# Kernel optimization log

Hardware: AMD Instinct MI355X
Metric: run time of the kernel (lower is better)

## Reference

```python
import jax, jax.numpy as jnp
import numpy as np

B, T, E = 2, 2048, 2048
H, D = 16, 128
KVH = H // 2
THETA = 10000.0

def make_rope(dim, seq_len, theta):
    inv_freqs = 1.0 / (theta ** (jnp.arange(0, dim, 2, dtype=jnp.float32) / dim))
    positions = jnp.arange(seq_len, dtype=jnp.float32)
    freqs = positions[:, None] * inv_freqs[None, :]  # (T, D/2)
    return jax.lax.complex(jnp.cos(freqs), jnp.sin(freqs))

def apply_rope(x, rope):
    # x: (B, h, T, D), rope: (T, D/2) complex
    xr = x.astype(jnp.float32).reshape(*x.shape[:-1], -1, 2)
    xc = jax.lax.complex(xr[..., 0], xr[..., 1])
    out = xc * rope[None, None, :, :]
    return jnp.stack([jnp.real(out), jnp.imag(out)], axis=-1).reshape(x.shape).astype(x.dtype)

def setup_inputs() -> dict:
    key = jax.random.key(0)
    ks = jax.random.split(key, 5)
    x = jax.random.normal(ks[0], (B, T, E), dtype=jnp.float32)
    mask = jnp.tril(jnp.ones((T, T), dtype=jnp.int32))[None, None]  # causal (1,1,T,T)
    s = 0.02
    wq = jax.random.normal(ks[1], (E, H * D), dtype=jnp.float32) * s
    wk = jax.random.normal(ks[2], (E, KVH * D), dtype=jnp.float32) * s
    wv = jax.random.normal(ks[3], (E, KVH * D), dtype=jnp.float32) * s
    wo = jax.random.normal(ks[4], (H * D, E), dtype=jnp.float32) * s
    return {"x": x, "mask": mask, "wq": wq, "wk": wk, "wv": wv, "wo": wo}

def reference(x, mask, wq, wk, wv, wo):
    rope = make_rope(D, T, THETA)
    q = (x @ wq).reshape(B, T, H, D).transpose(0, 2, 1, 3)      # (B,H,T,D)
    k = (x @ wk).reshape(B, T, KVH, D).transpose(0, 2, 1, 3)    # (B,KVH,T,D)
    v = (x @ wv).reshape(B, T, KVH, D).transpose(0, 2, 1, 3)
    q = apply_rope(q, rope)
    k = apply_rope(k, rope)
    # GQA: repeat kv heads to match query heads
    k = jnp.repeat(k, H // KVH, axis=1)
    v = jnp.repeat(v, H // KVH, axis=1)
    scale = D ** -0.5
    attn = jnp.einsum('bhqd,bhkd->bhqk', q, k) * scale
    attn = jnp.where(mask == 0, -jnp.inf, attn)
    attn = jax.nn.softmax(attn, axis=-1)
    attn = jnp.where(jnp.isnan(attn), 0.0, attn)
    out = jnp.einsum('bhqk,bhkd->bhqd', attn, v)
    out = out.transpose(0, 2, 1, 3).reshape(B, T, H * D)
    return out @ wo
```

## Files before the change

### kernel.cpp

```cpp
#include <hip/hip_runtime.h>
#include <math.h>

#define Bb   2
#define Tt   2048
#define Ee   2048
#define Hh   16
#define KVHh 8
#define Dd   128
#define Mm   (Bb*Tt)

typedef unsigned short u16;
typedef __bf16 bf16x8 __attribute__((ext_vector_type(8)));
typedef float  f32x4  __attribute__((ext_vector_type(4)));

__device__ __forceinline__ u16 f2b(float f) {
    union { float f; unsigned u; } v; v.f = f;
    unsigned r = v.u + 0x7fffu + ((v.u >> 16) & 1u);
    return (u16)(r >> 16);
}
__device__ __forceinline__ u16 f2b_fast(float f) {
    union { float f; unsigned u; } v; v.f = f;
    return (u16)((v.u + 0x8000u) >> 16);
}
__device__ __forceinline__ float b2f(u16 h) {
    union { float f; unsigned u; } v; v.u = ((unsigned)h) << 16;
    return v.f;
}

__device__ __forceinline__ void gl_lds16(const u16* g, u16* l) {
    __builtin_amdgcn_global_load_lds(
        (const __attribute__((address_space(1))) void*)g,
        (__attribute__((address_space(3))) void*)l,
        16, 0, 0);
}

__global__ void cast_x_kernel(const float* __restrict__ x, u16* __restrict__ xb, int n4) {
    int i = blockIdx.x * blockDim.x + threadIdx.x;
    if (i >= n4) return;
    float4 f = ((const float4*)x)[i];
    unsigned lo = (unsigned)f2b(f.x) | ((unsigned)f2b(f.y) << 16);
    unsigned hi = (unsigned)f2b(f.z) | ((unsigned)f2b(f.w) << 16);
    ((uint2*)xb)[i] = make_uint2(lo, hi);
}

__global__ void transpose_cast4_kernel(const float* __restrict__ wq, const float* __restrict__ wk,
                                       const float* __restrict__ wv, const float* __restrict__ wo,
                                       u16* __restrict__ btqkv, u16* __restrict__ bto) {
    __shared__ float tile[32][33];
    int job = blockIdx.z;
    const float* W; u16* Bt; int C;
    if (job == 0)      { W = wq; Bt = btqkv;                      C = 2048; }
    else if (job == 1) { W = wk; Bt = btqkv + (size_t)2048 * Ee;  C = 1024; }
    else if (job == 2) { W = wv; Bt = btqkv + (size_t)3072 * Ee;  C = 1024; }
    else               { W = wo; Bt = bto;                        C = 2048; }
    int c0 = blockIdx.x * 32, r0 = blockIdx.y * 32;
    if (c0 >= C) return;
    int x = threadIdx.x, y = threadIdx.y;
    for (int j = y; j < 32; j += 8)
        tile[j][x] = W[(size_t)(r0 + j) * C + c0 + x];
    __syncthreads();
    for (int j = y; j < 32; j += 8)
        Bt[(size_t)(c0 + j) * 2048 + r0 + x] = f2b(tile[x][j]);
}

__global__ void transpose_v_kernel(const u16* __restrict__ v, u16* __restrict__ vt) {
    __shared__ u16 tile[32][34];
    int x = threadIdx.x, y = threadIdx.y;
    int c0 = blockIdx.x * 32;
    int r0 = blockIdx.y * 32;
    int bk = blockIdx.z;
    for (int j = y; j < 32; j += 8)
        tile[j][x] = v[((size_t)bk * Tt + r0 + j) * Dd + c0 + x];
    __syncthreads();
    for (int j = y; j < 32; j += 8)
        vt[((size_t)bk * Dd + c0 + j) * Tt + r0 + x] = tile[x][j];
}

__global__ void rope_kernel(u16* __restrict__ q, u16* __restrict__ k) {
    const int QP = Bb * Hh * Tt * (Dd / 2);
    const int KP = Bb * KVHh * Tt * (Dd / 2);
    int idx = blockIdx.x * blockDim.x + threadIdx.x;
    if (idx >= QP + KP) return;
    u16* ptr; int p;
    if (idx < QP) { ptr = q; p = idx; } else { ptr = k; p = idx - QP; }
    int d2 = p & 63;
    int row = p >> 6;
    int t = row & (Tt - 1);
    float ex = (float)(2 * d2) * (1.0f / 128.0f);
    float inv = expf(-ex * 9.210340371976184f);
    float fr = (float)t * inv;
    float c = cosf(fr), s = sinf(fr);
    size_t e0 = (size_t)row * Dd + 2 * d2;
    unsigned pair = *(const unsigned*)(ptr + e0);
    float x0 = b2f((u16)(pair & 0xffff));
    float x1 = b2f((u16)(pair >> 16));
    float o0 = x0 * c - x1 * s;
    float o1 = x0 * s + x1 * c;
    *(unsigned*)(ptr + e0) = (unsigned)f2b(o0) | ((unsigned)f2b(o1) << 16);
}

__global__ __launch_bounds__(512, 2) void gemm8_kernel(
    const u16* __restrict__ A, const u16* __restrict__ Bt,
    int Ndim, int Kdim, int mode,
    u16* __restrict__ qo, u16* __restrict__ ko, u16* __restrict__ vo,
    float* __restrict__ fo)
{
    __shared__ u16 sm[2][2][256 * 64];
    const int tid = threadIdx.x;
    const int lane = tid & 63, w = tid >> 6;
    const int quad = lane >> 4, l15 = lane & 15;
    const int hl = (l15 >> 2) & 3;
    const int bn = blockIdx.x, bm = blockIdx.y;
    const int wm = (w >> 2) * 128, wn = (w & 3) * 64;
    const int rowA0 = bm * 256, rowB0 = bn * 256;

    const int srow = lane >> 3;
    const int sj4  = ((lane >> 5) & 1) << 4;
    const int scol = (lane & 7) * 8;
    const int wa = w & 3, wb = w >> 2;
    const int cAlo = (wm >> 3) + 2 * wa;
    const int cAhi = (wm >> 3) + 8 + 2 * wa;
    const int cBlo = (wn >> 3) + 2 * wb;
    const int cBhi = (wn >> 3) + 4 + 2 * wb;

    const int col0 = (quad * 8) ^ (hl << 4);
    const int col1 = (32 + quad * 8) ^ (hl << 4);

    f32x4 acc[8][4];
#pragma unroll
    for (int i = 0; i < 8; i++)
#pragma unroll
        for (int j = 0; j < 4; j++) acc[i][j] = (f32x4){0.f, 0.f, 0.f, 0.f};

#define STAGE_PAIR(G, Grow0, ldsb, cb, kk) do { \
    gl_lds16((G) + (size_t)((Grow0) + (cb) * 8 + srow) * Kdim + (kk) + (scol ^ sj4), \
             (ldsb) + (cb) * 512); \
    gl_lds16((G) + (size_t)((Grow0) + (cb) * 8 + 8 + srow) * Kdim + (kk) + (scol ^ sj4 ^ 32), \
             (ldsb) + (cb) * 512 + 512); \
} while (0)

    STAGE_PAIR(A,  rowA0, &sm[0][0][0], cAlo, 0);
    STAGE_PAIR(Bt, rowB0, &sm[0][1][0], cBlo, 0);
    STAGE_PAIR(Bt, rowB0, &sm[0][1][0], cBhi, 0);
    STAGE_PAIR(A,  rowA0, &sm[0][0][0], cAhi, 0);
    asm volatile("s_waitcnt vmcnt(4)" ::: "memory");
    __builtin_amdgcn_s_barrier();
    __builtin_amdgcn_sched_barrier(0);

    bf16x8 a4[4][2], bA[2][2], bB[2][2];
    const int NT = Kdim >> 6;

    for (int t = 0; t < NT; ++t) {
        u16* As = &sm[t & 1][0][0];
        u16* Bs = &sm[t & 1][1][0];
        u16* An = &sm[(t + 1) & 1][0][0];
        u16* Bn = &sm[(t + 1) & 1][1][0];
        const int kk = (t + 1) << 6;
        const bool st = (t + 1 < NT);

#pragma unroll
        for (int i = 0; i < 4; i++) {
            const u16* p = As + (wm + i * 16 + l15) * 64;
            a4[i][0] = *(const bf16x8*)(p + col0);
            a4[i][1] = *(const bf16x8*)(p + col1);
        }
#pragma unroll
        for (int j = 0; j < 2; j++) {
            const u16* p = Bs + (wn + j * 16 + l15) * 64;
            bA[j][0] = *(const bf16x8*)(p + col0);
            bA[j][1] = *(const bf16x8*)(p + col1);
        }
        if (st) STAGE_PAIR(A, rowA0, An, cAlo, kk);
        __builtin_amdgcn_sched_barrier(0);
        __builtin_amdgcn_s_barrier();
        __builtin_amdgcn_sched_barrier(0);
        __builtin_amdgcn_s_setprio(1);
#pragma unroll
        for (int kc = 0; kc < 2; kc++)
#pragma unroll
            for (int i = 0; i < 4; i++)
#pragma unroll
                for (int j = 0; j < 2; j++)
                    acc[i][j] = __builtin_amdgcn_mfma_f32_16x16x32_bf16(a4[i][kc], bA[j][kc], acc[i][j], 0, 0, 0);
        __builtin_amdgcn_s_setprio(0);
        __builtin_amdgcn_sched_barrier(0);
        if (st) { asm volatile("s_waitcnt vmcnt(4)" ::: "memory"); }
        else    { asm volatile("s_waitcnt vmcnt(2)" ::: "memory"); }
        __builtin_amdgcn_s_barrier();
        __builtin_amdgcn_sched_barrier(0);

#pragma unroll
        for (int j = 0; j < 2; j++) {
            const u16* p = Bs + (wn + 32 + j * 16 + l15) * 64;
            bB[j][0] = *(const bf16x8*)(p + col0);
            bB[j][1] = *(const bf16x8*)(p + col1);
        }
        if (st) STAGE_PAIR(Bt, rowB0, Bn, cBlo, kk);
        __builtin_amdgcn_sched_barrier(0);
        __builtin_amdgcn_s_barrier();
        __builtin_amdgcn_sched_barrier(0);
        __builtin_amdgcn_s_setprio(1);
#pragma unroll
        for (int kc = 0; kc < 2; kc++)
#pragma unroll
            for (int i = 0; i < 4; i++)
#pragma unroll
                for (int j = 0; j < 2; j++)
                    acc[i][j + 2] = __builtin_amdgcn_mfma_f32_16x16x32_bf16(a4[i][kc], bB[j][kc], acc[i][j + 2], 0, 0, 0);
        __builtin_amdgcn_s_setprio(0);
        __builtin_amdgcn_sched_barrier(0);
        if (st) { asm volatile("s_waitcnt vmcnt(4)" ::: "memory"); }
        else    { asm volatile("s_waitcnt vmcnt(0)" ::: "memory"); }
        __builtin_amdgcn_s_barrier();
        __builtin_amdgcn_sched_barrier(0);

#pragma unroll
        for (int i = 0; i < 4; i++) {
            const u16* p = As + (wm + 64 + i * 16 + l15) * 64;
            a4[i][0] = *(const bf16x8*)(p + col0);
            a4[i][1] = *(const bf16x8*)(p + col1);
        }
        if (st) STAGE_PAIR(Bt, rowB0, Bn, cBhi, kk);
        __builtin_amdgcn_sched_barrier(0);
        __builtin_amdgcn_s_barrier();
        __builtin_amdgcn_sched_barrier(0);
        __builtin_amdgcn_s_setprio(1);
#pragma unroll
        for (int kc = 0; kc < 2; kc++)
#pragma unroll
            for (int i = 0; i < 4; i++)
#pragma unroll
                for (int j = 0; j < 2; j++)
                    acc[i + 4][j] = __builtin_amdgcn_mfma_f32_16x16x32_bf16(a4[i][kc], bA[j][kc], acc[i + 4][j], 0, 0, 0);
        __builtin_amdgcn_s_setprio(0);
        __builtin_amdgcn_sched_barrier(0);
        if (st) { asm volatile("s_waitcnt vmcnt(4)" ::: "memory"); }
        __builtin_amdgcn_s_barrier();
        __builtin_amdgcn_sched_barrier(0);

        if (st) STAGE_PAIR(A, rowA0, An, cAhi, kk);
        __builtin_amdgcn_sched_barrier(0);
        __builtin_amdgcn_s_barrier();
        __builtin_amdgcn_sched_barrier(0);
        __builtin_amdgcn_s_setprio(1);
#pragma unroll
        for (int kc = 0; kc < 2; kc++)
#pragma unroll
            for (int i = 0; i < 4; i++)
#pragma unroll
                for (int j = 0; j < 2; j++)
                    acc[i + 4][j + 2] = __builtin_amdgcn_mfma_f32_16x16x32_bf16(a4[i][kc], bB[j][kc], acc[i + 4][j + 2], 0, 0, 0);
        __builtin_amdgcn_s_setprio(0);
        __builtin_amdgcn_sched_barrier(0);
        if (st) { asm volatile("s_waitcnt vmcnt(4)" ::: "memory"); }
        __builtin_amdgcn_s_barrier();
        __builtin_amdgcn_sched_barrier(0);
    }
#undef STAGE_PAIR

#pragma unroll
    for (int i = 0; i < 8; i++)
#pragma unroll
        for (int j = 0; j < 4; j++)
#pragma unroll
            for (int r = 0; r < 4; r++) {
                int m = rowA0 + wm + i * 16 + quad * 4 + r;
                int n = rowB0 + wn + j * 16 + l15;
                float val = acc[i][j][r];
                if (mode == 0) {
                    int b = m >> 11, tq = m & (Tt - 1);
                    if (n < 2048) {
                        int h = n >> 7, d = n & 127;
                        qo[(((size_t)(b * Hh + h)) * Tt + tq) * Dd + d] = f2b(val);
                    } else if (n < 3072) {
                        int h = (n - 2048) >> 7, d = n & 127;
                        ko[(((size_t)(b * KVHh + h)) * Tt + tq) * Dd + d] = f2b(val);
                    } else {
                        int h = (n - 3072) >> 7, d = n & 127;
                        vo[(((size_t)(b * KVHh + h)) * Tt + tq) * Dd + d] = f2b(val);
                    }
                } else {
                    fo[(size_t)m * Ndim + n] = val;
                }
            }
}

#define LDKV 136
#define LDVT 72
#define LDP  72

__global__ __launch_bounds__(256) void flash_kernel(
    const u16* __restrict__ q, const u16* __restrict__ k, const u16* __restrict__ vt,
    u16* __restrict__ attn)
{
    __shared__ u16 Ksh[64 * LDKV];
    __shared__ u16 Vtsh[128 * LDVT];
    __shared__ u16 Psh[128 * LDP];

    int tid = threadIdx.x, lane = tid & 63, w = tid >> 6;
    int quad = lane >> 4, l15 = lane & 15;
    int pr = blockIdx.x;
    int bh = blockIdx.y;
    int b = bh >> 4, h = bh & 15;
    int kvh = h >> 1;
    const u16* qbase = q + (size_t)bh * Tt * Dd;
    const u16* kbase = k + ((size_t)(b * KVHh + kvh)) * Tt * Dd;
    const u16* vtbase = vt + ((size_t)(b * KVHh + kvh)) * Dd * Tt;
    u16* P0 = Psh + (2 * w) * 16 * LDP;
    u16* P1 = Psh + (2 * w + 1) * 16 * LDP;
    const float sc2 = 0.08838834764831845f * 1.4426950408889634f;

    for (int half = 0; half < 2; half++) {
        int qt = half ? (15 - pr) : pr;
        int row0 = qt * 128 + w * 32;

        bf16x8 qf0[4], qf1[4];
        {
            const u16* qr0 = qbase + (size_t)(row0 + l15) * Dd + quad * 8;
            const u16* qr1 = qbase + (size_t)(row0 + 16 + l15) * Dd + quad * 8;
#pragma unroll
            for (int c = 0; c < 4; c++) {
                qf0[c] = *(const bf16x8*)(qr0 + c * 32);
                qf1[c] = *(const bf16x8*)(qr1 + c * 32);
            }
        }

        f32x4 o0[8], o1[8];
#pragma unroll
        for (int i = 0; i < 8; i++) { o0[i] = (f32x4){0.f,0.f,0.f,0.f}; o1[i] = (f32x4){0.f,0.f,0.f,0.f}; }
        float l0[4] = {0.f,0.f,0.f,0.f}, l1[4] = {0.f,0.f,0.f,0.f};

        int nkt = 2 * (qt + 1);
        for (int kt = 0; kt < nkt; kt++) {
#pragma unroll
            for (int j = 0; j < 4; j++) {
                int chunk = j * 256 + tid;
                int rk = chunk >> 4, ck = chunk & 15;
                uint4 dk = *(const uint4*)(kbase + (size_t)(kt * 64 + rk) * Dd + ck * 8);
                *(uint4*)(Ksh + rk * LDKV + ck * 8) = dk;
                int rv = chunk >> 3, cv = chunk & 7;
                uint4 dv = *(const uint4*)(vtbase + (size_t)rv * Tt + kt * 64 + cv * 8);
                *(uint4*)(Vtsh + rv * LDVT + cv * 8) = dv;
            }
            __syncthreads();

            bool skip = (kt * 64) > (row0 + 31);
            if (!skip) {
                f32x4 s0[4], s1[4];
#pragma unroll
                for (int ni = 0; ni < 4; ni++) { s0[ni] = (f32x4){0.f,0.f,0.f,0.f}; s1[ni] = (f32x4){0.f,0.f,0.f,0.f}; }
#pragma unroll
                for (int c = 0; c < 4; c++)
#pragma unroll
                    for (int ni = 0; ni < 4; ni++) {
                        bf16x8 kf = *(const bf16x8*)(Ksh + (ni * 16 + l15) * LDKV + c * 32 + quad * 8);
                        s0[ni] = __builtin_amdgcn_mfma_f32_16x16x32_bf16(qf0[c], kf, s0[ni], 0, 0, 0);
                        s1[ni] = __builtin_amdgcn_mfma_f32_16x16x32_bf16(qf1[c], kf, s1[ni], 0, 0, 0);
                    }

                if (kt * 64 + 63 > row0) {
#pragma unroll
                    for (int ni = 0; ni < 4; ni++)
#pragma unroll
                        for (int r = 0; r < 4; r++) {
                            int kcol = kt * 64 + ni * 16 + l15;
                            int qa = row0 + quad * 4 + r;
                            int qb2 = row0 + 16 + quad * 4 + r;
                            if (kcol > qa)  s0[ni][r] = -__builtin_inff();
                            if (kcol > qb2) s1[ni][r] = -__builtin_inff();
                        }
                }

#pragma unroll
                for (int ni = 0; ni < 4; ni++)
#pragma unroll
                    for (int r = 0; r < 4; r++) {
                        float p0 = exp2f(s0[ni][r] * sc2);
                        l0[r] += p0;
                        P0[(quad * 4 + r) * LDP + ni * 16 + l15] = f2b_fast(p0);
                        float p1 = exp2f(s1[ni][r] * sc2);
                        l1[r] += p1;
                        P1[(quad * 4 + r) * LDP + ni * 16 + l15] = f2b_fast(p1);
                    }
            }
            __syncthreads();

            if (!skip) {
#pragma unroll
                for (int c = 0; c < 2; c++) {
                    bf16x8 pf0 = *(const bf16x8*)(P0 + l15 * LDP + c * 32 + quad * 8);
                    bf16x8 pf1 = *(const bf16x8*)(P1 + l15 * LDP + c * 32 + quad * 8);
#pragma unroll
                    for (int di = 0; di < 8; di++) {
                        bf16x8 vf = *(const bf16x8*)(Vtsh + (di * 16 + l15) * LDVT + c * 32 + quad * 8);
                        o0[di] = __builtin_amdgcn_mfma_f32_16x16x32_bf16(pf0, vf, o0[di], 0, 0, 0);
                        o1[di] = __builtin_amdgcn_mfma_f32_16x16x32_bf16(pf1, vf, o1[di], 0, 0, 0);
                    }
                }
            }
            __syncthreads();
        }

        float linv0[4], linv1[4];
#pragma unroll
        for (int r = 0; r < 4; r++) {
            float a = l0[r];
            a += __shfl_xor(a, 1); a += __shfl_xor(a, 2);
            a += __shfl_xor(a, 4); a += __shfl_xor(a, 8);
            linv0[r] = 1.0f / a;
            float c2 = l1[r];
            c2 += __shfl_xor(c2, 1); c2 += __shfl_xor(c2, 2);
            c2 += __shfl_xor(c2, 4); c2 += __shfl_xor(c2, 8);
            linv1[r] = 1.0f / c2;
        }
#pragma unroll
        for (int di = 0; di < 8; di++)
#pragma unroll
            for (int r = 0; r < 4; r++) {
                int ta = row0 + quad * 4 + r;
                int tb = row0 + 16 + quad * 4 + r;
                size_t ma = (size_t)b * Tt + ta;
                size_t mb = (size_t)b * Tt + tb;
                attn[ma * (Hh * Dd) + h * Dd + di * 16 + l15] = f2b(o0[di][r] * linv0[r]);
                attn[mb * (Hh * Dd) + h * Dd + di * 16 + l15] = f2b(o1[di][r] * linv1[r]);
            }
        __syncthreads();
    }
}

extern "C" void kernel_launch(void* const* d_in, const int* in_sizes, int n_in,
                              void* d_out, int out_size, void* d_ws, size_t ws_size,
                              hipStream_t stream) {
    const float* x  = (const float*)d_in[0];
    const float* wq = (const float*)d_in[2];
    const float* wk = (const float*)d_in[3];
    const float* wv = (const float*)d_in[4];
    const float* wo = (const float*)d_in[5];
    float* out = (float*)d_out;

    char* ws = (char*)d_ws;
    u16* xb    = (u16*)ws; ws += (size_t)Mm * Ee * 2;
    u16* btqkv = (u16*)ws; ws += (size_t)4096 * Ee * 2;
    u16* bto   = (u16*)ws; ws += (size_t)Ee * (Hh * Dd) * 2;
    u16* qb    = (u16*)ws; ws += (size_t)Bb * Hh * Tt * Dd * 2;
    u16* kb    = (u16*)ws; ws += (size_t)Bb * KVHh * Tt * Dd * 2;
    u16* vb    = (u16*)ws; ws += (size_t)Bb * KVHh * Tt * Dd * 2;
    u16* vtb   = (u16*)ws; ws += (size_t)Bb * KVHh * Dd * Tt * 2;
    u16* attn  = (u16*)ws; ws += (size_t)Mm * (Hh * Dd) * 2;

    cast_x_kernel<<<(Mm * Ee / 4 + 255) / 256, 256, 0, stream>>>(x, xb, Mm * Ee / 4);

    transpose_cast4_kernel<<<dim3(64, 64, 4), dim3(32, 8), 0, stream>>>(wq, wk, wv, wo, btqkv, bto);

    gemm8_kernel<<<dim3(16, 16), 512, 0, stream>>>(xb, btqkv, 4096, Ee, 0,
                                                   qb, kb, vb, nullptr);

    {
        int total = Bb * Hh * Tt * 64 + Bb * KVHh * Tt * 64;
        rope_kernel<<<(total + 255) / 256, 256, 0, stream>>>(qb, kb);
    }

    transpose_v_kernel<<<dim3(Dd / 32, Tt / 32, Bb * KVHh), dim3(32, 8), 0, stream>>>(vb, vtb);

    flash_kernel<<<dim3(Tt / 256, Bb * Hh), 256, 0, stream>>>(qb, kb, vtb, attn);

    gemm8_kernel<<<dim3(8, 16), 512, 0, stream>>>(attn, bto, 2048, Hh * Dd, 1,
                                                  nullptr, nullptr, nullptr, out);
}
```

Before: 399.6 us.

## Split-K output projection and double-buffer K/V tiles in flash attention

The output projection GEMM is split along K into two halves on a z-grid dimension. The second half writes partial sums into reused scratch (the q buffer), and a new elementwise kernel adds them into the output. This raises the block count from 128 toward CU count, at the cost of extra memory traffic and a launch. The flash kernel now double-buffers K and V^T tiles in LDS, prefetching the next tile into registers during compute, and raises wave priority around the MFMA loops.

```diff
diff --git a/kernel.cpp b/kernel.cpp
--- a/kernel.cpp
+++ b/kernel.cpp
@@ -41,6 +41,15 @@
     unsigned lo = (unsigned)f2b(f.x) | ((unsigned)f2b(f.y) << 16);
     unsigned hi = (unsigned)f2b(f.z) | ((unsigned)f2b(f.w) << 16);
     ((uint2*)xb)[i] = make_uint2(lo, hi);
+}
+
+__global__ void addf4_kernel(float* __restrict__ o, const float* __restrict__ a, int n4) {
+    int i = blockIdx.x * blockDim.x + threadIdx.x;
+    if (i >= n4) return;
+    float4 x = ((const float4*)o)[i];
+    float4 y = ((const float4*)a)[i];
+    x.x += y.x; x.y += y.y; x.z += y.z; x.w += y.w;
+    ((float4*)o)[i] = x;
 }
 
 __global__ void transpose_cast4_kernel(const float* __restrict__ wq, const float* __restrict__ wk,
@@ -100,17 +109,19 @@
 }
 
 __global__ __launch_bounds__(512, 2) void gemm8_kernel(
-    const u16* __restrict__ A, const u16* __restrict__ Bt,
-    int Ndim, int Kdim, int mode,
+    const u16* __restrict__ A0, const u16* __restrict__ Bt0,
+    int Ndim, int Kdim, int Kstride, int mode,
     u16* __restrict__ qo, u16* __restrict__ ko, u16* __restrict__ vo,
-    float* __restrict__ fo)
+    float* __restrict__ fo, float* __restrict__ fo2)
 {
     __shared__ u16 sm[2][2][256 * 64];
     const int tid = threadIdx.x;
     const int lane = tid & 63, w = tid >> 6;
     const int quad = lane >> 4, l15 = lane & 15;
     const int hl = (l15 >> 2) & 3;
-    const int bn = blockIdx.x, bm = blockIdx.y;
+    const int bn = blockIdx.x, bm = blockIdx.y, kz = blockIdx.z;
+    const u16* A  = A0  + (size_t)kz * Kdim;
+    const u16* Bt = Bt0 + (size_t)kz * Kdim;
     const int wm = (w >> 2) * 128, wn = (w & 3) * 64;
     const int rowA0 = bm * 256, rowB0 = bn * 256;
 
@@ -133,9 +144,9 @@
         for (int j = 0; j < 4; j++) acc[i][j] = (f32x4){0.f, 0.f, 0.f, 0.f};
 
 #define STAGE_PAIR(G, Grow0, ldsb, cb, kk) do { \
-    gl_lds16((G) + (size_t)((Grow0) + (cb) * 8 + srow) * Kdim + (kk) + (scol ^ sj4), \
+    gl_lds16((G) + (size_t)((Grow0) + (cb) * 8 + srow) * Kstride + (kk) + (scol ^ sj4), \
              (ldsb) + (cb) * 512); \
-    gl_lds16((G) + (size_t)((Grow0) + (cb) * 8 + 8 + srow) * Kdim + (kk) + (scol ^ sj4 ^ 32), \
+    gl_lds16((G) + (size_t)((Grow0) + (cb) * 8 + 8 + srow) * Kstride + (kk) + (scol ^ sj4 ^ 32), \
              (ldsb) + (cb) * 512 + 512); \
 } while (0)
 
@@ -258,6 +269,7 @@
     }
 #undef STAGE_PAIR
 
+    float* ft = kz ? fo2 : fo;
 #pragma unroll
     for (int i = 0; i < 8; i++)
 #pragma unroll
@@ -280,7 +292,7 @@
                         vo[(((size_t)(b * KVHh + h)) * Tt + tq) * Dd + d] = f2b(val);
                     }
                 } else {
-                    fo[(size_t)m * Ndim + n] = val;
+                    ft[(size_t)m * Ndim + n] = val;
                 }
             }
 }
@@ -293,8 +305,8 @@
     const u16* __restrict__ q, const u16* __restrict__ k, const u16* __restrict__ vt,
     u16* __restrict__ attn)
 {
-    __shared__ u16 Ksh[64 * LDKV];
-    __shared__ u16 Vtsh[128 * LDVT];
+    __shared__ u16 Ksh[2][64 * LDKV];
+    __shared__ u16 Vtsh[2][128 * LDVT];
     __shared__ u16 Psh[128 * LDP];
 
     int tid = threadIdx.x, lane = tid & 63, w = tid >> 6;
@@ -310,6 +322,25 @@
     u16* P1 = Psh + (2 * w + 1) * 16 * LDP;
     const float sc2 = 0.08838834764831845f * 1.4426950408889634f;
 
+    const int krow = tid >> 4, kcol = (tid & 15) * 8;
+    const int vrow = tid >> 3, vcol = (tid & 7) * 8;
+    uint4 rk4[4], rv4[4];
+
+#define FL_LOAD(ktn) do { \
+    _Pragma("unroll") \
+    for (int j = 0; j < 4; j++) { \
+        rk4[j] = *(const uint4*)(kbase + (size_t)((ktn) * 64 + j * 16 + krow) * Dd + kcol); \
+        rv4[j] = *(const uint4*)(vtbase + (size_t)(j * 32 + vrow) * Tt + (ktn) * 64 + vcol); \
+    } \
+} while (0)
+#define FL_WRITE(bsel) do { \
+    _Pragma("unroll") \
+    for (int j = 0; j < 4; j++) { \
+        *(uint4*)(Ksh[bsel] + (j * 16 + krow) * LDKV + kcol) = rk4[j]; \
+        *(uint4*)(Vtsh[bsel] + (j * 32 + vrow) * LDVT + vcol) = rv4[j]; \
+    } \
+} while (0)
+
     for (int half = 0; half < 2; half++) {
         int qt = half ? (15 - pr) : pr;
         int row0 = qt * 128 + w * 32;
@@ -331,43 +362,44 @@
         float l0[4] = {0.f,0.f,0.f,0.f}, l1[4] = {0.f,0.f,0.f,0.f};
 
         int nkt = 2 * (qt + 1);
+
+        FL_LOAD(0);
+        FL_WRITE(0);
+        __syncthreads();
+
         for (int kt = 0; kt < nkt; kt++) {
-#pragma unroll
-            for (int j = 0; j < 4; j++) {
-                int chunk = j * 256 + tid;
-                int rk = chunk >> 4, ck = chunk & 15;
-                uint4 dk = *(const uint4*)(kbase + (size_t)(kt * 64 + rk) * Dd + ck * 8);
-                *(uint4*)(Ksh + rk * LDKV + ck * 8) = dk;
-                int rv = chunk >> 3, cv = chunk & 7;
-                uint4 dv = *(const uint4*)(vtbase + (size_t)rv * Tt + kt * 64 + cv * 8);
-                *(uint4*)(Vtsh + rv * LDVT + cv * 8) = dv;
-            }
-            __syncthreads();
+            const int cur = kt & 1, nxt = cur ^ 1;
+            const bool pf = (kt + 1 < nkt);
+            if (pf) FL_LOAD(kt + 1);
+            const u16* Kc = Ksh[cur];
+            const u16* Vc = Vtsh[cur];
 
             bool skip = (kt * 64) > (row0 + 31);
             if (!skip) {
                 f32x4 s0[4], s1[4];
 #pragma unroll
                 for (int ni = 0; ni < 4; ni++) { s0[ni] = (f32x4){0.f,0.f,0.f,0.f}; s1[ni] = (f32x4){0.f,0.f,0.f,0.f}; }
+                __builtin_amdgcn_s_setprio(1);
 #pragma unroll
                 for (int c = 0; c < 4; c++)
 #pragma unroll
                     for (int ni = 0; ni < 4; ni++) {
-                        bf16x8 kf = *(const bf16x8*)(Ksh + (ni * 16 + l15) * LDKV + c * 32 + quad * 8);
+                        bf16x8 kf = *(const bf16x8*)(Kc + (ni * 16 + l15) * LDKV + c * 32 + quad * 8);
                         s0[ni] = __builtin_amdgcn_mfma_f32_16x16x32_bf16(qf0[c], kf, s0[ni], 0, 0, 0);
                         s1[ni] = __builtin_amdgcn_mfma_f32_16x16x32_bf16(qf1[c], kf, s1[ni], 0, 0, 0);
                     }
+                __builtin_amdgcn_s_setprio(0);
 
                 if (kt * 64 + 63 > row0) {
 #pragma unroll
                     for (int ni = 0; ni < 4; ni++)
 #pragma unroll
                         for (int r = 0; r < 4; r++) {
-                            int kcol = kt * 64 + ni * 16 + l15;
+                            int kcolm = kt * 64 + ni * 16 + l15;
                             int qa = row0 + quad * 4 + r;
                             int qb2 = row0 + 16 + quad * 4 + r;
-                            if (kcol > qa)  s0[ni][r] = -__builtin_inff();
-                            if (kcol > qb2) s1[ni][r] = -__builtin_inff();
+                            if (kcolm > qa)  s0[ni][r] = -__builtin_inff();
+                            if (kcolm > qb2) s1[ni][r] = -__builtin_inff();
                         }
                 }
 
@@ -385,18 +417,22 @@
             }
             __syncthreads();
 
+            if (pf) FL_WRITE(nxt);
+
             if (!skip) {
+                __builtin_amdgcn_s_setprio(1);
 #pragma unroll
                 for (int c = 0; c < 2; c++) {
                     bf16x8 pf0 = *(const bf16x8*)(P0 + l15 * LDP + c * 32 + quad * 8);
                     bf16x8 pf1 = *(const bf16x8*)(P1 + l15 * LDP + c * 32 + quad * 8);
 #pragma unroll
                     for (int di = 0; di < 8; di++) {
-                        bf16x8 vf = *(const bf16x8*)(Vtsh + (di * 16 + l15) * LDVT + c * 32 + quad * 8);
+                        bf16x8 vf = *(const bf16x8*)(Vc + (di * 16 + l15) * LDVT + c * 32 + quad * 8);
                         o0[di] = __builtin_amdgcn_mfma_f32_16x16x32_bf16(pf0, vf, o0[di], 0, 0, 0);
                         o1[di] = __builtin_amdgcn_mfma_f32_16x16x32_bf16(pf1, vf, o1[di], 0, 0, 0);
                     }
                 }
+                __builtin_amdgcn_s_setprio(0);
             }
             __syncthreads();
         }
@@ -424,8 +460,9 @@
                 attn[ma * (Hh * Dd) + h * Dd + di * 16 + l15] = f2b(o0[di][r] * linv0[r]);
                 attn[mb * (Hh * Dd) + h * Dd + di * 16 + l15] = f2b(o1[di][r] * linv1[r]);
             }
-        __syncthreads();
     }
+#undef FL_LOAD
+#undef FL_WRITE
 }
 
 extern "C" void kernel_launch(void* const* d_in, const int* in_sizes, int n_in,
@@ -448,12 +485,14 @@
     u16* vtb   = (u16*)ws; ws += (size_t)Bb * KVHh * Dd * Tt * 2;
     u16* attn  = (u16*)ws; ws += (size_t)Mm * (Hh * Dd) * 2;
 
+    float* fo2 = (float*)qb;
+
     cast_x_kernel<<<(Mm * Ee / 4 + 255) / 256, 256, 0, stream>>>(x, xb, Mm * Ee / 4);
 
     transpose_cast4_kernel<<<dim3(64, 64, 4), dim3(32, 8), 0, stream>>>(wq, wk, wv, wo, btqkv, bto);
 
-    gemm8_kernel<<<dim3(16, 16), 512, 0, stream>>>(xb, btqkv, 4096, Ee, 0,
-                                                   qb, kb, vb, nullptr);
+    gemm8_kernel<<<dim3(16, 16, 1), 512, 0, stream>>>(xb, btqkv, 4096, Ee, Ee, 0,
+                                                      qb, kb, vb, nullptr, nullptr);
 
     {
         int total = Bb * Hh * Tt * 64 + Bb * KVHh * Tt * 64;
@@ -464,6 +503,7 @@
 
     flash_kernel<<<dim3(Tt / 256, Bb * Hh), 256, 0, stream>>>(qb, kb, vtb, attn);
 
-    gemm8_kernel<<<dim3(8, 16), 512, 0, stream>>>(attn, bto, 2048, Hh * Dd, 1,
-                                                  nullptr, nullptr, nullptr, out);
-}
+    gemm8_kernel<<<dim3(8, 16, 2), 512, 0, stream>>>(attn, bto, 2048, (Hh * Dd) / 2, Hh * Dd, 1,
+                                                     nullptr, nullptr, nullptr, out, fo2);
+    addf4_kernel<<<(Mm * Ee / 4 + 255) / 256, 256, 0, stream>>>(out, fo2, Mm * Ee / 4);
+}
```

New measurement: 426.0 us. 1.07x slower.

## Split-K output projection and split flash blocks per query tile

Applied to the files above, without the earlier changes.

The output projection GEMM now runs as a two-way split-K over a z grid dimension. Its second partial goes into the freed q buffer and is added back by a separate float4 add kernel. The flash kernel no longer loops over two paired query tiles per block. Each block now handles one tile, which doubles the grid and sets launch bounds to 2 blocks per CU, to raise occupancy and fill more CUs. The cost is an extra 32 MB of fp32 traffic for the partial sum and the add pass, plus some loss of causal load pairing.

```diff
diff --git a/kernel.cpp b/kernel.cpp
--- a/kernel.cpp
+++ b/kernel.cpp
@@ -41,6 +41,15 @@
     unsigned lo = (unsigned)f2b(f.x) | ((unsigned)f2b(f.y) << 16);
     unsigned hi = (unsigned)f2b(f.z) | ((unsigned)f2b(f.w) << 16);
     ((uint2*)xb)[i] = make_uint2(lo, hi);
+}
+
+__global__ void addf4_kernel(float* __restrict__ o, const float* __restrict__ a, int n4) {
+    int i = blockIdx.x * blockDim.x + threadIdx.x;
+    if (i >= n4) return;
+    float4 x = ((const float4*)o)[i];
+    float4 y = ((const float4*)a)[i];
+    x.x += y.x; x.y += y.y; x.z += y.z; x.w += y.w;
+    ((float4*)o)[i] = x;
 }
 
 __global__ void transpose_cast4_kernel(const float* __restrict__ wq, const float* __restrict__ wk,
@@ -100,17 +109,19 @@
 }
 
 __global__ __launch_bounds__(512, 2) void gemm8_kernel(
-    const u16* __restrict__ A, const u16* __restrict__ Bt,
-    int Ndim, int Kdim, int mode,
+    const u16* __restrict__ A0, const u16* __restrict__ Bt0,
+    int Ndim, int Kdim, int Kstride, int mode,
     u16* __restrict__ qo, u16* __restrict__ ko, u16* __restrict__ vo,
-    float* __restrict__ fo)
+    float* __restrict__ fo, float* __restrict__ fo2)
 {
     __shared__ u16 sm[2][2][256 * 64];
     const int tid = threadIdx.x;
     const int lane = tid & 63, w = tid >> 6;
     const int quad = lane >> 4, l15 = lane & 15;
     const int hl = (l15 >> 2) & 3;
-    const int bn = blockIdx.x, bm = blockIdx.y;
+    const int bn = blockIdx.x, bm = blockIdx.y, kz = blockIdx.z;
+    const u16* A  = A0  + (size_t)kz * Kdim;
+    const u16* Bt = Bt0 + (size_t)kz * Kdim;
     const int wm = (w >> 2) * 128, wn = (w & 3) * 64;
     const int rowA0 = bm * 256, rowB0 = bn * 256;
 
@@ -133,9 +144,9 @@
         for (int j = 0; j < 4; j++) acc[i][j] = (f32x4){0.f, 0.f, 0.f, 0.f};
 
 #define STAGE_PAIR(G, Grow0, ldsb, cb, kk) do { \
-    gl_lds16((G) + (size_t)((Grow0) + (cb) * 8 + srow) * Kdim + (kk) + (scol ^ sj4), \
+    gl_lds16((G) + (size_t)((Grow0) + (cb) * 8 + srow) * Kstride + (kk) + (scol ^ sj4), \
              (ldsb) + (cb) * 512); \
-    gl_lds16((G) + (size_t)((Grow0) + (cb) * 8 + 8 + srow) * Kdim + (kk) + (scol ^ sj4 ^ 32), \
+    gl_lds16((G) + (size_t)((Grow0) + (cb) * 8 + 8 + srow) * Kstride + (kk) + (scol ^ sj4 ^ 32), \
              (ldsb) + (cb) * 512 + 512); \
 } while (0)
 
@@ -258,6 +269,7 @@
     }
 #undef STAGE_PAIR
 
+    float* ft = kz ? fo2 : fo;
 #pragma unroll
     for (int i = 0; i < 8; i++)
 #pragma unroll
@@ -280,7 +292,7 @@
                         vo[(((size_t)(b * KVHh + h)) * Tt + tq) * Dd + d] = f2b(val);
                     }
                 } else {
-                    fo[(size_t)m * Ndim + n] = val;
+                    ft[(size_t)m * Ndim + n] = val;
                 }
             }
 }
@@ -289,7 +301,7 @@
 #define LDVT 72
 #define LDP  72
 
-__global__ __launch_bounds__(256) void flash_kernel(
+__global__ __launch_bounds__(256, 2) void flash_kernel(
     const u16* __restrict__ q, const u16* __restrict__ k, const u16* __restrict__ vt,
     u16* __restrict__ attn)
 {
@@ -299,8 +311,10 @@
 
     int tid = threadIdx.x, lane = tid & 63, w = tid >> 6;
     int quad = lane >> 4, l15 = lane & 15;
-    int pr = blockIdx.x;
-    int bh = blockIdx.y;
+    int flat = blockIdx.y * gridDim.x + blockIdx.x;
+    int i5 = flat & 255, hi = flat >> 8;
+    int bh = i5 >> 3, p = i5 & 7;
+    int qt = hi ? p : 15 - p;
     int b = bh >> 4, h = bh & 15;
     int kvh = h >> 1;
     const u16* qbase = q + (size_t)bh * Tt * Dd;
@@ -310,122 +324,118 @@
     u16* P1 = Psh + (2 * w + 1) * 16 * LDP;
     const float sc2 = 0.08838834764831845f * 1.4426950408889634f;
 
-    for (int half = 0; half < 2; half++) {
-        int qt = half ? (15 - pr) : pr;
-        int row0 = qt * 128 + w * 32;
-
-        bf16x8 qf0[4], qf1[4];
-        {
-            const u16* qr0 = qbase + (size_t)(row0 + l15) * Dd + quad * 8;
-            const u16* qr1 = qbase + (size_t)(row0 + 16 + l15) * Dd + quad * 8;
-#pragma unroll
-            for (int c = 0; c < 4; c++) {
-                qf0[c] = *(const bf16x8*)(qr0 + c * 32);
-                qf1[c] = *(const bf16x8*)(qr1 + c * 32);
-            }
-        }
-
-        f32x4 o0[8], o1[8];
-#pragma unroll
-        for (int i = 0; i < 8; i++) { o0[i] = (f32x4){0.f,0.f,0.f,0.f}; o1[i] = (f32x4){0.f,0.f,0.f,0.f}; }
-        float l0[4] = {0.f,0.f,0.f,0.f}, l1[4] = {0.f,0.f,0.f,0.f};
-
-        int nkt = 2 * (qt + 1);
-        for (int kt = 0; kt < nkt; kt++) {
-#pragma unroll
-            for (int j = 0; j < 4; j++) {
-                int chunk = j * 256 + tid;
-                int rk = chunk >> 4, ck = chunk & 15;
-                uint4 dk = *(const uint4*)(kbase + (size_t)(kt * 64 + rk) * Dd + ck * 8);
-                *(uint4*)(Ksh + rk * LDKV + ck * 8) = dk;
-                int rv = chunk >> 3, cv = chunk & 7;
-                uint4 dv = *(const uint4*)(vtbase + (size_t)rv * Tt + kt * 64 + cv * 8);
-                *(uint4*)(Vtsh + rv * LDVT + cv * 8) = dv;
-            }
-            __syncthreads();
-
-            bool skip = (kt * 64) > (row0 + 31);
-            if (!skip) {
-                f32x4 s0[4], s1[4];
-#pragma unroll
-                for (int ni = 0; ni < 4; ni++) { s0[ni] = (f32x4){0.f,0.f,0.f,0.f}; s1[ni] = (f32x4){0.f,0.f,0.f,0.f}; }
-#pragma unroll
-                for (int c = 0; c < 4; c++)
-#pragma unroll
-                    for (int ni = 0; ni < 4; ni++) {
-                        bf16x8 kf = *(const bf16x8*)(Ksh + (ni * 16 + l15) * LDKV + c * 32 + quad * 8);
-                        s0[ni] = __builtin_amdgcn_mfma_f32_16x16x32_bf16(qf0[c], kf, s0[ni], 0, 0, 0);
-                        s1[ni] = __builtin_amdgcn_mfma_f32_16x16x32_bf16(qf1[c], kf, s1[ni], 0, 0, 0);
-                    }
-
-                if (kt * 64 + 63 > row0) {
-#pragma unroll
-                    for (int ni = 0; ni < 4; ni++)
-#pragma unroll
-                        for (int r = 0; r < 4; r++) {
-                            int kcol = kt * 64 + ni * 16 + l15;
-                            int qa = row0 + quad * 4 + r;
-                            int qb2 = row0 + 16 + quad * 4 + r;
-                            if (kcol > qa)  s0[ni][r] = -__builtin_inff();
-                            if (kcol > qb2) s1[ni][r] = -__builtin_inff();
-                        }
+    int row0 = qt * 128 + w * 32;
+
+    bf16x8 qf0[4], qf1[4];
+    {
+        const u16* qr0 = qbase + (size_t)(row0 + l15) * Dd + quad * 8;
+        const u16* qr1 = qbase + (size_t)(row0 + 16 + l15) * Dd + quad * 8;
+#pragma unroll
+        for (int c = 0; c < 4; c++) {
+            qf0[c] = *(const bf16x8*)(qr0 + c * 32);
+            qf1[c] = *(const bf16x8*)(qr1 + c * 32);
+        }
+    }
+
+    f32x4 o0[8], o1[8];
+#pragma unroll
+    for (int i = 0; i < 8; i++) { o0[i] = (f32x4){0.f,0.f,0.f,0.f}; o1[i] = (f32x4){0.f,0.f,0.f,0.f}; }
+    float l0[4] = {0.f,0.f,0.f,0.f}, l1[4] = {0.f,0.f,0.f,0.f};
+
+    int nkt = 2 * (qt + 1);
+    for (int kt = 0; kt < nkt; kt++) {
+#pragma unroll
+        for (int j = 0; j < 4; j++) {
+            int chunk = j * 256 + tid;
+            int rk = chunk >> 4, ck = chunk & 15;
+            uint4 dk = *(const uint4*)(kbase + (size_t)(kt * 64 + rk) * Dd + ck * 8);
+            *(uint4*)(Ksh + rk * LDKV + ck * 8) = dk;
+            int rv = chunk >> 3, cv = chunk & 7;
+            uint4 dv = *(const uint4*)(vtbase + (size_t)rv * Tt + kt * 64 + cv * 8);
+            *(uint4*)(Vtsh + rv * LDVT + cv * 8) = dv;
+        }
+        __syncthreads();
+
+        bool skip = (kt * 64) > (row0 + 31);
+        if (!skip) {
+            f32x4 s0[4], s1[4];
+#pragma unroll
+            for (int ni = 0; ni < 4; ni++) { s0[ni] = (f32x4){0.f,0.f,0.f,0.f}; s1[ni] = (f32x4){0.f,0.f,0.f,0.f}; }
+#pragma unroll
+            for (int c = 0; c < 4; c++)
+#pragma unroll
+                for (int ni = 0; ni < 4; ni++) {
+                    bf16x8 kf = *(const bf16x8*)(Ksh + (ni * 16 + l15) * LDKV + c * 32 + quad * 8);
+                    s0[ni] = __builtin_amdgcn_mfma_f32_16x16x32_bf16(qf0[c], kf, s0[ni], 0, 0, 0);
+                    s1[ni] = __builtin_amdgcn_mfma_f32_16x16x32_bf16(qf1[c], kf, s1[ni], 0, 0, 0);
                 }
 
+            if (kt * 64 + 63 > row0) {
 #pragma unroll
                 for (int ni = 0; ni < 4; ni++)
 #pragma unroll
                     for (int r = 0; r < 4; r++) {
-                        float p0 = exp2f(s0[ni][r] * sc2);
-                        l0[r] += p0;
-                        P0[(quad * 4 + r) * LDP + ni * 16 + l15] = f2b_fast(p0);
-                        float p1 = exp2f(s1[ni][r] * sc2);
-                        l1[r] += p1;
-                        P1[(quad * 4 + r) * LDP + ni * 16 + l15] = f2b_fast(p1);
+                        int kcol = kt * 64 + ni * 16 + l15;
+                        int qa = row0 + quad * 4 + r;
+                        int qb2 = row0 + 16 + quad * 4 + r;
+                        if (kcol > qa)  s0[ni][r] = -__builtin_inff();
+                        if (kcol > qb2) s1[ni][r] = -__builtin_inff();
                     }
             }
-            __syncthreads();
-
-            if (!skip) {
-#pragma unroll
-                for (int c = 0; c < 2; c++) {
-                    bf16x8 pf0 = *(const bf16x8*)(P0 + l15 * LDP + c * 32 + quad * 8);
-                    bf16x8 pf1 = *(const bf16x8*)(P1 + l15 * LDP + c * 32 + quad * 8);
-#pragma unroll
-                    for (int di = 0; di < 8; di++) {
-                        bf16x8 vf = *(const bf16x8*)(Vtsh + (di * 16 + l15) * LDVT + c * 32 + quad * 8);
-                        o0[di] = __builtin_amdgcn_mfma_f32_16x16x32_bf16(pf0, vf, o0[di], 0, 0, 0);
-                        o1[di] = __builtin_amdgcn_mfma_f32_16x16x32_bf16(pf1, vf, o1[di], 0, 0, 0);
-                    }
+
+#pragma unroll
+            for (int ni = 0; ni < 4; ni++)
+#pragma unroll
+                for (int r = 0; r < 4; r++) {
+                    float p0 = exp2f(s0[ni][r] * sc2);
+                    l0[r] += p0;
+                    P0[(quad * 4 + r) * LDP + ni * 16 + l15] = f2b_fast(p0);
+                    float p1 = exp2f(s1[ni][r] * sc2);
+                    l1[r] += p1;
+                    P1[(quad * 4 + r) * LDP + ni * 16 + l15] = f2b_fast(p1);
+                }
+        }
+        __syncthreads();
+
+        if (!skip) {
+#pragma unroll
+            for (int c = 0; c < 2; c++) {
+                bf16x8 pf0 = *(const bf16x8*)(P0 + l15 * LDP + c * 32 + quad * 8);
+                bf16x8 pf1 = *(const bf16x8*)(P1 + l15 * LDP + c * 32 + quad * 8);
+#pragma unroll
+                for (int di = 0; di < 8; di++) {
+                    bf16x8 vf = *(const bf16x8*)(Vtsh + (di * 16 + l15) * LDVT + c * 32 + quad * 8);
+                    o0[di] = __builtin_amdgcn_mfma_f32_16x16x32_bf16(pf0, vf, o0[di], 0, 0, 0);
+                    o1[di] = __builtin_amdgcn_mfma_f32_16x16x32_bf16(pf1, vf, o1[di], 0, 0, 0);
                 }
             }
-            __syncthreads();
-        }
-
-        float linv0[4], linv1[4];
-#pragma unroll
-        for (int r = 0; r < 4; r++) {
-            float a = l0[r];
-            a += __shfl_xor(a, 1); a += __shfl_xor(a, 2);
-            a += __shfl_xor(a, 4); a += __shfl_xor(a, 8);
-            linv0[r] = 1.0f / a;
-            float c2 = l1[r];
-            c2 += __shfl_xor(c2, 1); c2 += __shfl_xor(c2, 2);
-            c2 += __shfl_xor(c2, 4); c2 += __shfl_xor(c2, 8);
-            linv1[r] = 1.0f / c2;
-        }
-#pragma unroll
-        for (int di = 0; di < 8; di++)
-#pragma unroll
-            for (int r = 0; r < 4; r++) {
-                int ta = row0 + quad * 4 + r;
-                int tb = row0 + 16 + quad * 4 + r;
-                size_t ma = (size_t)b * Tt + ta;
-                size_t mb = (size_t)b * Tt + tb;
-                attn[ma * (Hh * Dd) + h * Dd + di * 16 + l15] = f2b(o0[di][r] * linv0[r]);
-                attn[mb * (Hh * Dd) + h * Dd + di * 16 + l15] = f2b(o1[di][r] * linv1[r]);
-            }
+        }
         __syncthreads();
     }
+
+    float linv0[4], linv1[4];
+#pragma unroll
+    for (int r = 0; r < 4; r++) {
+        float a = l0[r];
+        a += __shfl_xor(a, 1); a += __shfl_xor(a, 2);
+        a += __shfl_xor(a, 4); a += __shfl_xor(a, 8);
+        linv0[r] = 1.0f / a;
+        float c2 = l1[r];
+        c2 += __shfl_xor(c2, 1); c2 += __shfl_xor(c2, 2);
+        c2 += __shfl_xor(c2, 4); c2 += __shfl_xor(c2, 8);
+        linv1[r] = 1.0f / c2;
+    }
+#pragma unroll
+    for (int di = 0; di < 8; di++)
+#pragma unroll
+        for (int r = 0; r < 4; r++) {
+            int ta = row0 + quad * 4 + r;
+            int tb = row0 + 16 + quad * 4 + r;
+            size_t ma = (size_t)b * Tt + ta;
+            size_t mb = (size_t)b * Tt + tb;
+            attn[ma * (Hh * Dd) + h * Dd + di * 16 + l15] = f2b(o0[di][r] * linv0[r]);
+            attn[mb * (Hh * Dd) + h * Dd + di * 16 + l15] = f2b(o1[di][r] * linv1[r]);
+        }
 }
 
 extern "C" void kernel_launch(void* const* d_in, const int* in_sizes, int n_in,
@@ -448,12 +458,14 @@
     u16* vtb   = (u16*)ws; ws += (size_t)Bb * KVHh * Dd * Tt * 2;
     u16* attn  = (u16*)ws; ws += (size_t)Mm * (Hh * Dd) * 2;
 
+    float* fo2 = (float*)qb;
+
     cast_x_kernel<<<(Mm * Ee / 4 + 255) / 256, 256, 0, stream>>>(x, xb, Mm * Ee / 4);
 
     transpose_cast4_kernel<<<dim3(64, 64, 4), dim3(32, 8), 0, stream>>>(wq, wk, wv, wo, btqkv, bto);
 
-    gemm8_kernel<<<dim3(16, 16), 512, 0, stream>>>(xb, btqkv, 4096, Ee, 0,
-                                                   qb, kb, vb, nullptr);
+    gemm8_kernel<<<dim3(16, 16, 1), 512, 0, stream>>>(xb, btqkv, 4096, Ee, Ee, 0,
+                                                      qb, kb, vb, nullptr, nullptr);
 
     {
         int total = Bb * Hh * Tt * 64 + Bb * KVHh * Tt * 64;
@@ -462,8 +474,9 @@
 
     transpose_v_kernel<<<dim3(Dd / 32, Tt / 32, Bb * KVHh), dim3(32, 8), 0, stream>>>(vb, vtb);
 
-    flash_kernel<<<dim3(Tt / 256, Bb * Hh), 256, 0, stream>>>(qb, kb, vtb, attn);
-
-    gemm8_kernel<<<dim3(8, 16), 512, 0, stream>>>(attn, bto, 2048, Hh * Dd, 1,
-                                                  nullptr, nullptr, nullptr, out);
-}
+    flash_kernel<<<dim3(16, 32), 256, 0, stream>>>(qb, kb, vtb, attn);
+
+    gemm8_kernel<<<dim3(8, 16, 2), 512, 0, stream>>>(attn, bto, 2048, (Hh * Dd) / 2, Hh * Dd, 1,
+                                                     nullptr, nullptr, nullptr, out, fo2);
+    addf4_kernel<<<(Mm * Ee / 4 + 255) / 256, 256, 0, stream>>>(out, fo2, Mm * Ee / 4);
+}
```

New measurement: 433.8 us. 8.5% more time.
